# Kernel optimization log

Measured on AMD Instinct MI355X. Metric: run time of the kernel, lower is better.

## Reference

```python
import jax, jax.numpy as jnp
import numpy as np


def setup_inputs() -> dict:
    key = jax.random.key(0)
    k1, k2 = jax.random.split(key)
    N, D, G = 200000, 256, 512
    x = jax.random.normal(k1, (N, D), dtype=jnp.float32)
    batch_ids = jnp.sort(jax.random.randint(k2, (N,), 0, G, dtype=jnp.int64))
    return {"x": x, "batch_ids": batch_ids, "num_graphs": G}


def reference(x, batch_ids, num_graphs):
    # Segment-mean: equivalent to the per-graph masked mean loop.
    sums = jax.ops.segment_sum(x, batch_ids, num_segments=num_graphs)  # [G, D]
    counts = jax.ops.segment_sum(jnp.ones((x.shape[0],), dtype=x.dtype),
                                 batch_ids, num_segments=num_graphs)  # [G]
    graph_features = sums / counts[:, None]
    return graph_features
```

## Files before the change

### kernel.cpp

```cpp
#include <hip/hip_runtime.h>


__global__ __launch_bounds__(256) void segmean_kernel(
    const float* __restrict__ x,
    const int*   __restrict__ ids,
    float*       __restrict__ out,
    int N, int D)
{
    const int g = (int)blockIdx.x;

    int lo = 0, hi = N;
    while (lo < hi) {
        int mid = (lo + hi) >> 1;
        if (ids[mid] < g) lo = mid + 1; else hi = mid;
    }
    const int start = lo;
    hi = N;
    while (lo < hi) {
        int mid = (lo + hi) >> 1;
        if (ids[mid] <= g) lo = mid + 1; else hi = mid;
    }
    const int end = lo;
    const int count = end - start;

    const int tpr    = D >> 2;
    const int rpi    = (int)blockDim.x / tpr;
    const int t      = (int)threadIdx.x;
    const int rowoff = t / tpr;
    const int col    = (t % tpr) << 2;

    float4 acc = make_float4(0.f, 0.f, 0.f, 0.f);
    #pragma unroll 4
    for (int r = start + rowoff; r < end; r += rpi) {
        const float4 v = *reinterpret_cast<const float4*>(x + (size_t)r * (size_t)D + col);
        acc.x += v.x; acc.y += v.y; acc.z += v.z; acc.w += v.w;
    }

    __shared__ float4 sdata[256];
    sdata[t] = acc;
    __syncthreads();

    if (t < tpr) {
        float4 s = sdata[t];
        for (int k = 1; k < rpi; ++k) {
            const float4 v = sdata[t + k * tpr];
            s.x += v.x; s.y += v.y; s.z += v.z; s.w += v.w;
        }
        const float c = (float)count;
        const float4 o = make_float4(s.x / c, s.y / c, s.z / c, s.w / c);
        *reinterpret_cast<float4*>(out + (size_t)g * (size_t)D + col) = o;
    }
}

extern "C" void kernel_launch(void* const* d_in, const int* in_sizes, int n_in,
                              void* d_out, int out_size, void* d_ws, size_t ws_size,
                              hipStream_t stream) {
    const float* x   = (const float*)d_in[0];
    const int*   ids = (const int*)d_in[1];
    float*       out = (float*)d_out;

    const int N = in_sizes[1];
    const int D = in_sizes[0] / N;
    const int G = out_size / D;

    dim3 grid(G), block(256);
    segmean_kernel<<<grid, block, 0, stream>>>(x, ids, out, N, D);
}
```

Before: 41.03 us.

## Split each segment across four column-slice blocks with interleaved binary searches

Launches four blocks per graph, each reducing a quarter of the feature columns, so the grid grows from G to 4G blocks and fills the GPU better. The two boundary binary searches are interleaved in one loop to overlap their dependent loads. The reduction uses wave shuffles plus a small shared array, and the divide becomes a reciprocal multiply. Each row read now covers only 64 floats per block, which shortens contiguous accesses, and the search work is repeated four times per graph. The code assumes D=256 (16 threads per row slice).

```diff
diff --git a/kernel.cpp b/kernel.cpp
--- a/kernel.cpp
+++ b/kernel.cpp
@@ -1,5 +1,7 @@
 #include <hip/hip_runtime.h>
 
+
+#define SLICES 4
 
 __global__ __launch_bounds__(256) void segmean_kernel(
     const float* __restrict__ x,
@@ -7,47 +9,61 @@
     float*       __restrict__ out,
     int N, int D)
 {
-    const int g = (int)blockIdx.x;
+    const int bid = (int)blockIdx.x;
+    const int g   = bid >> 2;
+    const int s   = bid & 3;
 
-    int lo = 0, hi = N;
-    while (lo < hi) {
-        int mid = (lo + hi) >> 1;
-        if (ids[mid] < g) lo = mid + 1; else hi = mid;
+    int lo0 = 0, hi0 = N, lo1 = 0, hi1 = N;
+    while ((lo0 < hi0) | (lo1 < hi1)) {
+        if (lo0 < hi0) {
+            const int m = (lo0 + hi0) >> 1;
+            if (ids[m] <  g) lo0 = m + 1; else hi0 = m;
+        }
+        if (lo1 < hi1) {
+            const int m = (lo1 + hi1) >> 1;
+            if (ids[m] <= g) lo1 = m + 1; else hi1 = m;
+        }
     }
-    const int start = lo;
-    hi = N;
-    while (lo < hi) {
-        int mid = (lo + hi) >> 1;
-        if (ids[mid] <= g) lo = mid + 1; else hi = mid;
-    }
-    const int end = lo;
+    const int start = lo0;
+    const int end   = lo1;
     const int count = end - start;
 
-    const int tpr    = D >> 2;
+    const int Dslice = D >> 2;
+    const int tpr    = Dslice >> 2;
     const int rpi    = (int)blockDim.x / tpr;
     const int t      = (int)threadIdx.x;
     const int rowoff = t / tpr;
-    const int col    = (t % tpr) << 2;
+    const int col    = s * Dslice + (t % tpr) * 4;
 
     float4 acc = make_float4(0.f, 0.f, 0.f, 0.f);
-    #pragma unroll 4
+    #pragma unroll 2
     for (int r = start + rowoff; r < end; r += rpi) {
         const float4 v = *reinterpret_cast<const float4*>(x + (size_t)r * (size_t)D + col);
         acc.x += v.x; acc.y += v.y; acc.z += v.z; acc.w += v.w;
     }
 
-    __shared__ float4 sdata[256];
-    sdata[t] = acc;
+    acc.x += __shfl_xor(acc.x, 16); acc.y += __shfl_xor(acc.y, 16);
+    acc.z += __shfl_xor(acc.z, 16); acc.w += __shfl_xor(acc.w, 16);
+    acc.x += __shfl_xor(acc.x, 32); acc.y += __shfl_xor(acc.y, 32);
+    acc.z += __shfl_xor(acc.z, 32); acc.w += __shfl_xor(acc.w, 32);
+
+    __shared__ float4 sdata[4][16];
+    const int wave = t >> 6;
+    const int lane = t & 63;
+    if (lane < 16) sdata[wave][lane] = acc;
     __syncthreads();
 
     if (t < tpr) {
-        float4 s = sdata[t];
-        for (int k = 1; k < rpi; ++k) {
-            const float4 v = sdata[t + k * tpr];
-            s.x += v.x; s.y += v.y; s.z += v.z; s.w += v.w;
-        }
-        const float c = (float)count;
-        const float4 o = make_float4(s.x / c, s.y / c, s.z / c, s.w / c);
+        const float4 a = sdata[0][t];
+        const float4 b = sdata[1][t];
+        const float4 c = sdata[2][t];
+        const float4 d = sdata[3][t];
+        const float inv = 1.0f / (float)count;
+        float4 o;
+        o.x = ((a.x + b.x) + (c.x + d.x)) * inv;
+        o.y = ((a.y + b.y) + (c.y + d.y)) * inv;
+        o.z = ((a.z + b.z) + (c.z + d.z)) * inv;
+        o.w = ((a.w + b.w) + (c.w + d.w)) * inv;
         *reinterpret_cast<float4*>(out + (size_t)g * (size_t)D + col) = o;
     }
 }
@@ -63,6 +79,6 @@
     const int D = in_sizes[0] / N;
     const int G = out_size / D;
 
-    dim3 grid(G), block(256);
+    dim3 grid(G * SLICES), block(256);
     segmean_kernel<<<grid, block, 0, stream>>>(x, ids, out, N, D);
 }
```

Result: no change. 41.77 us (+1.8%).

## Split each segment across four blocks with a separate combine kernel

Applied to the files above, without the earlier changes.

Each graph segment is now reduced by four blocks that write partial sums to workspace, and a second kernel combines them and divides by the count. This raises block count to improve memory-level parallelism and CU occupancy. Boundary search first tries a narrow window around the expected uniform-distribution position, with a full-range fallback, and finds both bounds in one interleaved loop. It costs an extra launch plus workspace traffic, and hardcodes D=256 and a split of four.

```diff
diff --git a/kernel.cpp b/kernel.cpp
--- a/kernel.cpp
+++ b/kernel.cpp
@@ -1,54 +1,90 @@
 #include <hip/hip_runtime.h>
 
 
-__global__ __launch_bounds__(256) void segmean_kernel(
+#define SPLIT 4
+
+__global__ __launch_bounds__(256) void segmean_partial(
     const float* __restrict__ x,
     const int*   __restrict__ ids,
-    float*       __restrict__ out,
-    int N, int D)
+    float*       __restrict__ part,
+    int*         __restrict__ cnts,
+    int N, int D, int G)
 {
-    const int g = (int)blockIdx.x;
+    const int bid = (int)blockIdx.x;
+    const int g   = bid >> 2;
+    const int q   = bid & 3;
 
-    int lo = 0, hi = N;
-    while (lo < hi) {
-        int mid = (lo + hi) >> 1;
-        if (ids[mid] < g) lo = mid + 1; else hi = mid;
+    const int W  = 4096;
+    const int v0 = g, v1 = g + 1;
+    const long long c0 = (long long)v0 * N / G;
+    const long long c1 = (long long)v1 * N / G;
+    int lo0 = (int)(c0 - W < 0 ? 0 : c0 - W);
+    int hi0 = (int)(c0 + W > N ? N : c0 + W);
+    int lo1 = (int)(c1 - W < 0 ? 0 : c1 - W);
+    int hi1 = (int)(c1 + W > N ? N : c1 + W);
+    const bool ok0 = (lo0 == 0 || ids[lo0 - 1] < v0) && (hi0 == N || ids[hi0] >= v0);
+    const bool ok1 = (lo1 == 0 || ids[lo1 - 1] < v1) && (hi1 == N || ids[hi1] >= v1);
+    if (!ok0) { lo0 = 0; hi0 = N; }
+    if (!ok1) { lo1 = 0; hi1 = N; }
+    while ((lo0 < hi0) | (lo1 < hi1)) {
+        if (lo0 < hi0) {
+            const int m = (lo0 + hi0) >> 1;
+            if (ids[m] < v0) lo0 = m + 1; else hi0 = m;
+        }
+        if (lo1 < hi1) {
+            const int m = (lo1 + hi1) >> 1;
+            if (ids[m] < v1) lo1 = m + 1; else hi1 = m;
+        }
     }
-    const int start = lo;
-    hi = N;
-    while (lo < hi) {
-        int mid = (lo + hi) >> 1;
-        if (ids[mid] <= g) lo = mid + 1; else hi = mid;
-    }
-    const int end = lo;
+    const int start = lo0, end = lo1;
     const int count = end - start;
 
-    const int tpr    = D >> 2;
-    const int rpi    = (int)blockDim.x / tpr;
+    const int chunk = (count + SPLIT - 1) >> 2;
+    const int r0 = start + q * chunk;
+    const int r1 = (r0 + chunk < end) ? (r0 + chunk) : end;
+
     const int t      = (int)threadIdx.x;
-    const int rowoff = t / tpr;
-    const int col    = (t % tpr) << 2;
+    const int rowoff = t >> 6;
+    const int col    = (t & 63) << 2;
 
     float4 acc = make_float4(0.f, 0.f, 0.f, 0.f);
     #pragma unroll 4
-    for (int r = start + rowoff; r < end; r += rpi) {
+    for (int r = r0 + rowoff; r < r1; r += 4) {
         const float4 v = *reinterpret_cast<const float4*>(x + (size_t)r * (size_t)D + col);
         acc.x += v.x; acc.y += v.y; acc.z += v.z; acc.w += v.w;
     }
 
-    __shared__ float4 sdata[256];
-    sdata[t] = acc;
+    __shared__ float4 sd[256];
+    sd[t] = acc;
     __syncthreads();
 
-    if (t < tpr) {
-        float4 s = sdata[t];
-        for (int k = 1; k < rpi; ++k) {
-            const float4 v = sdata[t + k * tpr];
-            s.x += v.x; s.y += v.y; s.z += v.z; s.w += v.w;
-        }
-        const float c = (float)count;
-        const float4 o = make_float4(s.x / c, s.y / c, s.z / c, s.w / c);
-        *reinterpret_cast<float4*>(out + (size_t)g * (size_t)D + col) = o;
+    if (t < 64) {
+        const float4 a = sd[t];
+        const float4 b = sd[t + 64];
+        const float4 c = sd[t + 128];
+        const float4 d = sd[t + 192];
+        float4 s;
+        s.x = (a.x + b.x) + (c.x + d.x);
+        s.y = (a.y + b.y) + (c.y + d.y);
+        s.z = (a.z + b.z) + (c.z + d.z);
+        s.w = (a.w + b.w) + (c.w + d.w);
+        *reinterpret_cast<float4*>(part + (size_t)bid * (size_t)D + col) = s;
+    }
+    if (q == 0 && t == 0) cnts[g] = count;
+}
+
+__global__ __launch_bounds__(256) void segmean_combine(
+    const float* __restrict__ part,
+    const int*   __restrict__ cnts,
+    float*       __restrict__ out,
+    int D)
+{
+    const int g = (int)blockIdx.x;
+    const float inv = 1.0f / (float)cnts[g];
+    const float* p = part + (size_t)g * SPLIT * (size_t)D;
+    for (int d = (int)threadIdx.x; d < D; d += (int)blockDim.x) {
+        const float s = (p[d] + p[d + D]) + (p[d + 2 * D] + p[d + 3 * D]);
+        out[(size_t)g * (size_t)D + d] = s * inv;
     }
 }
 
@@ -63,6 +99,9 @@
     const int D = in_sizes[0] / N;
     const int G = out_size / D;
 
-    dim3 grid(G), block(256);
-    segmean_kernel<<<grid, block, 0, stream>>>(x, ids, out, N, D);
+    float* part = (float*)d_ws;
+    int*   cnts = (int*)((char*)d_ws + (size_t)G * SPLIT * D * sizeof(float));
+
+    segmean_partial<<<dim3(G * SPLIT), dim3(256), 0, stream>>>(x, ids, part, cnts, N, D, G);
+    segmean_combine<<<dim3(G), dim3(256), 0, stream>>>(part, cnts, out, D);
 }
```

Result: slower. 43.38 us (+5.7%).
